# Performance work log

Measured on AMD Instinct MI355X. Metric: run time of the kernel, lower is better.

## Reference

```python
import jax, jax.numpy as jnp
import numpy as np

BATCH = 131072
FEAS = 256
K = 256
DEPTH = 3


def setup_inputs() -> dict:
    key = jax.random.key(0)
    ks = jax.random.split(key, 16)
    # deep tower dims: k//1 -> k//2 -> k//3 -> k//4  == 256 -> 128 -> 85 -> 64
    dims = [K // i for i in range(1, DEPTH + 2)]
    inp = {
        "x": jax.random.normal(ks[0], (BATCH, FEAS), jnp.float32),
        "w_wide": jax.random.normal(ks[1], (FEAS, 1), jnp.float32) * 0.02,
        "b_wide": jnp.zeros((1,), jnp.float32),
        # nn.Parameter(torch.rand(feas, k)) -> uniform [0,1)
        "V": jax.random.uniform(ks[2], (FEAS, K), jnp.float32),
    }
    for i in range(DEPTH):
        fan_in, fan_out = dims[i], dims[i + 1]
        inp[f"w{i+1}"] = jax.random.normal(ks[3 + 2 * i], (fan_in, fan_out), jnp.float32) * (1.0 / np.sqrt(fan_in))
        inp[f"b{i+1}"] = jnp.zeros((fan_out,), jnp.float32)
    inp["w_out"] = jax.random.normal(ks[12], (dims[-1], 1), jnp.float32) * (1.0 / np.sqrt(dims[-1]))
    inp["b_out"] = jnp.zeros((1,), jnp.float32)
    return inp


def reference(x, w_wide, b_wide, V, w1, b1, w2, b2, w3, b3, w_out, b_out):
    # wide (linear) part: [B, 1]
    linear = x @ w_wide + b_wide
    # FM bi-interaction pooling. Original loop: sum_{j >= i} x_i x_j (v_i * v_j)
    # (break/continue on zeros only skip zero-valued terms). Including the
    # diagonal, this equals 0.5 * ((x @ V)^2 + (x^2) @ (V^2)).  [B, K]
    xv = x @ V
    x2v2 = (x * x) @ (V * V)
    tmp = 0.5 * (xv * xv + x2v2)
    # deep tower: Linear + ReLU at each depth
    for w, b in ((w1, b1), (w2, b2), (w3, b3)):
        tmp = jax.nn.relu(tmp @ w + b)
    deep_out = tmp @ w_out + b_out  # [B, 1]
    return jax.nn.sigmoid(linear + deep_out)
```

## Files before the change

### kernel.cpp

```cpp
#include <hip/hip_runtime.h>
#include <math.h>


typedef _Float16 f16;
typedef _Float16 f16x4 __attribute__((ext_vector_type(4)));
typedef _Float16 f16x8 __attribute__((ext_vector_type(8)));
typedef float f32x4 __attribute__((ext_vector_type(4)));

#define NROWS   131072
#define ROWS    64
#define FDIM    256
#define KDIM    256
#define D1      128
#define D2      85
#define D2P     96

#define OFF_VT_H   0x0UL
#define OFF_VT_L   0x20000UL
#define OFF_V2T    0x40000UL
#define OFF_W1T_H  0x60000UL
#define OFF_W1T_L  0x70000UL
#define OFF_W2T_H  0x80000UL
#define OFF_W2T_L  0x86000UL
#define OFF_W3T_H  0x8C000UL
#define OFF_W3T_L  0x8F000UL

static __device__ __forceinline__ f32x4 mfma16(f16x8 a, f16x8 b, f32x4 c) {
  return __builtin_amdgcn_mfma_f32_16x16x32_f16(a, b, c, 0, 0, 0);
}

__global__ __launch_bounds__(256) void prep_kernel(
    const float* __restrict__ V, const float* __restrict__ w1,
    const float* __restrict__ w2, const float* __restrict__ w3,
    f16* VT_h, f16* VT_l, f16* V2T,
    f16* W1T_h, f16* W1T_l, f16* W2T_h, f16* W2T_l, f16* W3T_h, f16* W3T_l) {
  int idx0 = blockIdx.x * 256 + threadIdx.x;
  int stride = gridDim.x * 256;
  for (int idx = idx0; idx < KDIM * FDIM; idx += stride) {
    int k = idx >> 8, i = idx & 255;
    float v = V[i * KDIM + k];
    f16 h = (f16)v;
    VT_h[idx] = h;
    VT_l[idx] = (f16)(v - (float)h);
    V2T[idx] = (f16)(v * v);
  }
  for (int idx = idx0; idx < D1 * KDIM; idx += stride) {
    int n = idx >> 8, k = idx & 255;
    float w = w1[k * D1 + n];
    f16 h = (f16)w;
    W1T_h[idx] = h;
    W1T_l[idx] = (f16)(w - (float)h);
  }
  for (int idx = idx0; idx < D2P * D1; idx += stride) {
    int n = idx >> 7, k = idx & 127;
    float w = (n < D2) ? w2[k * D2 + n] : 0.f;
    f16 h = (f16)w;
    W2T_h[idx] = h;
    W2T_l[idx] = (f16)(w - (float)h);
  }
  for (int idx = idx0; idx < 64 * D2P; idx += stride) {
    int n = idx / D2P, k = idx - n * D2P;
    float w = (k < D2) ? w3[k * 64 + n] : 0.f;
    f16 h = (f16)w;
    W3T_h[idx] = h;
    W3T_l[idx] = (f16)(w - (float)h);
  }
}

__global__ __launch_bounds__(512, 4) void fused_kernel(
    const float* __restrict__ x, const float* __restrict__ w_wide,
    const float* __restrict__ b_wide,
    const f16* __restrict__ VT_h, const f16* __restrict__ VT_l,
    const f16* __restrict__ V2T,
    const f16* __restrict__ W1T_h, const f16* __restrict__ W1T_l,
    const float* __restrict__ b1,
    const f16* __restrict__ W2T_h, const f16* __restrict__ W2T_l,
    const float* __restrict__ b2,
    const f16* __restrict__ W3T_h, const f16* __restrict__ W3T_l,
    const float* __restrict__ b3,
    const float* __restrict__ w_out, const float* __restrict__ b_out,
    float* __restrict__ out) {
  __shared__ __align__(16) f16 smem[32768];
  __shared__ float linS[ROWS];
  __shared__ float pfS[ROWS * 2];

  f16* tmpH = smem;
  f16* tmpL = smem + 16384;
  f16* sXh  = smem;
  f16* sXl  = smem + 2560;
  f16* sX2  = smem + 5120;
  f16* h1H  = smem + 16384;
  f16* h1L  = smem + 24576;
  f16* h2H  = smem;
  f16* h2L  = smem + 8192;

  const int tid = threadIdx.x;
  const int lane = tid & 63, wv = tid >> 6;
  const int q = lane >> 4, ln = lane & 15;
  const int row0 = blockIdx.x * ROWS;
  const int sr = tid >> 3, sc = (tid & 7) * 4;

  f32x4 accV[4][2], acc2[4][2];
#pragma unroll
  for (int i = 0; i < 4; ++i)
#pragma unroll
    for (int j = 0; j < 2; ++j) {
      accV[i][j] = (f32x4){0.f, 0.f, 0.f, 0.f};
      acc2[i][j] = (f32x4){0.f, 0.f, 0.f, 0.f};
    }
  float linp = 0.f;

  const float* xrow = x + (size_t)(row0 + sr) * FDIM + sc;
  float4 a_cur = *(const float4*)(xrow);
  float4 w_cur = *(const float4*)(w_wide + sc);

  for (int ks = 0; ks < 8; ++ks) {
    const int k0 = ks * 32;
    __syncthreads();
    {
      float f0[4] = {a_cur.x, a_cur.y, a_cur.z, a_cur.w};
      f16x4 h0, l0, q0;
#pragma unroll
      for (int j = 0; j < 4; ++j) {
        f16 h = (f16)f0[j];
        h0[j] = h;
        l0[j] = (f16)(f0[j] - (float)h);
        q0[j] = (f16)(f0[j] * f0[j]);
      }
      int off0 = sr * 40 + sc;
      *(f16x4*)(sXh + off0) = h0;
      *(f16x4*)(sXl + off0) = l0;
      *(f16x4*)(sX2 + off0) = q0;
    }
    __syncthreads();

    float4 a_nxt = a_cur, w_nxt = w_cur;
    if (ks < 7) {
      a_nxt = *(const float4*)(xrow + k0 + 32);
      w_nxt = *(const float4*)(w_wide + k0 + 32 + sc);
    }
    linp += a_cur.x * w_cur.x + a_cur.y * w_cur.y + a_cur.z * w_cur.z +
            a_cur.w * w_cur.w;

    f16x8 Bh[2], Bl[2], B2[2];
#pragma unroll
    for (int ni = 0; ni < 2; ++ni) {
      int n = wv * 32 + ni * 16 + ln;
      size_t boff = (size_t)n * FDIM + k0 + q * 8;
      Bh[ni] = *(const f16x8*)(VT_h + boff);
      Bl[ni] = *(const f16x8*)(VT_l + boff);
      B2[ni] = *(const f16x8*)(V2T + boff);
    }
#pragma unroll
    for (int mi = 0; mi < 4; ++mi) {
      int off = (mi * 16 + ln) * 40 + q * 8;
      f16x8 Ah = *(const f16x8*)(sXh + off);
      f16x8 Al = *(const f16x8*)(sXl + off);
      f16x8 A2 = *(const f16x8*)(sX2 + off);
#pragma unroll
      for (int ni = 0; ni < 2; ++ni) {
        accV[mi][ni] = mfma16(Al, Bh[ni], accV[mi][ni]);
        accV[mi][ni] = mfma16(Ah, Bl[ni], accV[mi][ni]);
        accV[mi][ni] = mfma16(Ah, Bh[ni], accV[mi][ni]);
        acc2[mi][ni] = mfma16(A2, B2[ni], acc2[mi][ni]);
      }
    }
    a_cur = a_nxt;
    w_cur = w_nxt;
  }

  {
    float s0 = linp;
    s0 += __shfl_xor(s0, 1);
    s0 += __shfl_xor(s0, 2);
    s0 += __shfl_xor(s0, 4);
    if ((tid & 7) == 0) linS[sr] = s0 + b_wide[0];
  }

  __syncthreads();

#pragma unroll
  for (int mi = 0; mi < 4; ++mi)
#pragma unroll
    for (int r = 0; r < 4; ++r) {
      int m = mi * 16 + q * 4 + r;
      int mrow = m * 256, msw = m & 7;
#pragma unroll
      for (int ni = 0; ni < 2; ++ni) {
        int n = wv * 32 + ni * 16 + ln;
        float xv = accV[mi][ni][r];
        float val = 0.5f * (xv * xv + acc2[mi][ni][r]);
        f16 hi = (f16)val;
        f16 lo = (f16)(val - (float)hi);
        int off = mrow + (((n >> 3) ^ msw) << 3) + (n & 7);
        tmpH[off] = hi;
        tmpL[off] = lo;
      }
    }

  __syncthreads();

  f32x4 acc1[4];
#pragma unroll
  for (int i = 0; i < 4; ++i) acc1[i] = (f32x4){0.f, 0.f, 0.f, 0.f};

#pragma unroll
  for (int ks = 0; ks < 8; ++ks) {
    size_t boff = (size_t)(wv * 16 + ln) * KDIM + ks * 32 + q * 8;
    f16x8 Bh = *(const f16x8*)(W1T_h + boff);
    f16x8 Bl = *(const f16x8*)(W1T_l + boff);
#pragma unroll
    for (int mi = 0; mi < 4; ++mi) {
      int m = mi * 16 + ln;
      int aoff = m * 256 + (((ks * 4 + q) ^ (m & 7)) << 3);
      f16x8 Ah = *(const f16x8*)(tmpH + aoff);
      f16x8 Al = *(const f16x8*)(tmpL + aoff);
      acc1[mi] = mfma16(Al, Bh, acc1[mi]);
      acc1[mi] = mfma16(Ah, Bl, acc1[mi]);
      acc1[mi] = mfma16(Ah, Bh, acc1[mi]);
    }
  }

  __syncthreads();

  {
    int n = wv * 16 + ln;
    float bias = b1[n];
#pragma unroll
    for (int mi = 0; mi < 4; ++mi)
#pragma unroll
      for (int r = 0; r < 4; ++r) {
        int m = mi * 16 + q * 4 + r;
        float z = acc1[mi][r] + bias;
        z = z > 0.f ? z : 0.f;
        f16 hi = (f16)z;
        f16 lo = (f16)(z - (float)hi);
        int off = m * 128 + (((n >> 3) ^ (m & 7)) << 3) + (n & 7);
        h1H[off] = hi;
        h1L[off] = lo;
      }
  }

  __syncthreads();

  const int mt = wv & 3, half = wv >> 2;
  f32x4 accL2[3];
#pragma unroll
  for (int j = 0; j < 3; ++j) accL2[j] = (f32x4){0.f, 0.f, 0.f, 0.f};

#pragma unroll
  for (int ks = 0; ks < 4; ++ks) {
    int m = mt * 16 + ln;
    int aoff = m * 128 + (((ks * 4 + q) ^ (m & 7)) << 3);
    f16x8 Ah = *(const f16x8*)(h1H + aoff);
    f16x8 Al = *(const f16x8*)(h1L + aoff);
#pragma unroll
    for (int nj = 0; nj < 3; ++nj) {
      int n = (half * 3 + nj) * 16 + ln;
      size_t boff = (size_t)n * D1 + ks * 32 + q * 8;
      f16x8 Bh = *(const f16x8*)(W2T_h + boff);
      f16x8 Bl = *(const f16x8*)(W2T_l + boff);
      accL2[nj] = mfma16(Al, Bh, accL2[nj]);
      accL2[nj] = mfma16(Ah, Bl, accL2[nj]);
      accL2[nj] = mfma16(Ah, Bh, accL2[nj]);
    }
  }

#pragma unroll
  for (int r = 0; r < 4; ++r) {
    int m = mt * 16 + q * 4 + r;
    int mrow = m * 128, msw = m & 7;
#pragma unroll
    for (int nj = 0; nj < 3; ++nj) {
      int n = (half * 3 + nj) * 16 + ln;
      float z = accL2[nj][r] + ((n < D2) ? b2[n] : 0.f);
      z = z > 0.f ? z : 0.f;
      f16 hi = (f16)z;
      f16 lo = (f16)(z - (float)hi);
      int off = mrow + (((n >> 3) ^ msw) << 3) + (n & 7);
      h2H[off] = hi;
      h2L[off] = lo;
    }
  }

  __syncthreads();

  f32x4 accL3[2];
  accL3[0] = (f32x4){0.f, 0.f, 0.f, 0.f};
  accL3[1] = (f32x4){0.f, 0.f, 0.f, 0.f};

#pragma unroll
  for (int ks = 0; ks < 3; ++ks) {
    int m = mt * 16 + ln;
    int aoff = m * 128 + (((ks * 4 + q) ^ (m & 7)) << 3);
    f16x8 Ah = *(const f16x8*)(h2H + aoff);
    f16x8 Al = *(const f16x8*)(h2L + aoff);
#pragma unroll
    for (int nj = 0; nj < 2; ++nj) {
      int n = (half * 2 + nj) * 16 + ln;
      size_t boff = (size_t)n * D2P + ks * 32 + q * 8;
      f16x8 Bh = *(const f16x8*)(W3T_h + boff);
      f16x8 Bl = *(const f16x8*)(W3T_l + boff);
      accL3[nj] = mfma16(Al, Bh, accL3[nj]);
      accL3[nj] = mfma16(Ah, Bl, accL3[nj]);
      accL3[nj] = mfma16(Ah, Bh, accL3[nj]);
    }
  }

  {
    float b3v[2], wov[2];
#pragma unroll
    for (int nj = 0; nj < 2; ++nj) {
      int n = (half * 2 + nj) * 16 + ln;
      b3v[nj] = b3[n];
      wov[nj] = w_out[n];
    }
#pragma unroll
    for (int r = 0; r < 4; ++r) {
      float part = 0.f;
#pragma unroll
      for (int nj = 0; nj < 2; ++nj) {
        float z = accL3[nj][r] + b3v[nj];
        part += (z > 0.f ? z : 0.f) * wov[nj];
      }
      part += __shfl_xor(part, 1);
      part += __shfl_xor(part, 2);
      part += __shfl_xor(part, 4);
      part += __shfl_xor(part, 8);
      if (ln == 0) pfS[(mt * 16 + q * 4 + r) * 2 + half] = part;
    }
  }

  __syncthreads();

  if (tid < ROWS) {
    float zf = linS[tid] + pfS[tid * 2] + pfS[tid * 2 + 1] + b_out[0];
    out[row0 + tid] = 1.f / (1.f + expf(-zf));
  }
}

extern "C" void kernel_launch(void* const* d_in, const int* in_sizes, int n_in,
                              void* d_out, int out_size, void* d_ws, size_t ws_size,
                              hipStream_t stream) {
  const float* x = (const float*)d_in[0];
  const float* w_wide = (const float*)d_in[1];
  const float* b_wide = (const float*)d_in[2];
  const float* V = (const float*)d_in[3];
  const float* w1 = (const float*)d_in[4];
  const float* b1 = (const float*)d_in[5];
  const float* w2 = (const float*)d_in[6];
  const float* b2 = (const float*)d_in[7];
  const float* w3 = (const float*)d_in[8];
  const float* b3 = (const float*)d_in[9];
  const float* w_out = (const float*)d_in[10];
  const float* b_out = (const float*)d_in[11];
  float* out = (float*)d_out;
  char* ws = (char*)d_ws;

  f16* VT_h = (f16*)(ws + OFF_VT_H);
  f16* VT_l = (f16*)(ws + OFF_VT_L);
  f16* V2T = (f16*)(ws + OFF_V2T);
  f16* W1T_h = (f16*)(ws + OFF_W1T_H);
  f16* W1T_l = (f16*)(ws + OFF_W1T_L);
  f16* W2T_h = (f16*)(ws + OFF_W2T_H);
  f16* W2T_l = (f16*)(ws + OFF_W2T_L);
  f16* W3T_h = (f16*)(ws + OFF_W3T_H);
  f16* W3T_l = (f16*)(ws + OFF_W3T_L);

  prep_kernel<<<64, 256, 0, stream>>>(V, w1, w2, w3, VT_h, VT_l, V2T, W1T_h,
                                      W1T_l, W2T_h, W2T_l, W3T_h, W3T_l);

  fused_kernel<<<NROWS / ROWS, 512, 0, stream>>>(
      x, w_wide, b_wide, VT_h, VT_l, V2T, W1T_h, W1T_l, b1, W2T_h, W2T_l, b2,
      W3T_h, W3T_l, b3, w_out, b_out, out);
}
```

Baseline: 405.0 us.

## Stage x in 128-wide K chunks to cut barriers in first GEMM

```diff
diff --git a/kernel.cpp b/kernel.cpp
--- a/kernel.cpp
+++ b/kernel.cpp
@@ -14,6 +14,8 @@
 #define D1      128
 #define D2      85
 #define D2P     96
+
+#define SSTRIDE 136
 
 #define OFF_VT_H   0x0UL
 #define OFF_VT_L   0x20000UL
@@ -84,11 +86,11 @@
   __shared__ float linS[ROWS];
   __shared__ float pfS[ROWS * 2];
 
+  f16* sXh  = smem;
+  f16* sXl  = smem + 8704;
+  f16* sX2  = smem + 17408;
   f16* tmpH = smem;
   f16* tmpL = smem + 16384;
-  f16* sXh  = smem;
-  f16* sXl  = smem + 2560;
-  f16* sX2  = smem + 5120;
   f16* h1H  = smem + 16384;
   f16* h1L  = smem + 24576;
   f16* h2H  = smem;
@@ -98,7 +100,7 @@
   const int lane = tid & 63, wv = tid >> 6;
   const int q = lane >> 4, ln = lane & 15;
   const int row0 = blockIdx.x * ROWS;
-  const int sr = tid >> 3, sc = (tid & 7) * 4;
+  const int sr = tid >> 3, sc = (tid & 7) * 16;
 
   f32x4 accV[4][2], acc2[4][2];
 #pragma unroll
@@ -110,15 +112,22 @@
     }
   float linp = 0.f;
 
-  const float* xrow = x + (size_t)(row0 + sr) * FDIM + sc;
-  float4 a_cur = *(const float4*)(xrow);
-  float4 w_cur = *(const float4*)(w_wide + sc);
-
-  for (int ks = 0; ks < 8; ++ks) {
-    const int k0 = ks * 32;
+  for (int kk = 0; kk < 2; ++kk) {
+    const int kbase = kk * 128;
+    float4 a[4], w4[4];
+    const float* xp = x + (size_t)(row0 + sr) * FDIM + kbase + sc;
+    const float* wp = w_wide + kbase + sc;
+#pragma unroll
+    for (int t = 0; t < 4; ++t) {
+      a[t] = *(const float4*)(xp + t * 4);
+      w4[t] = *(const float4*)(wp + t * 4);
+    }
     __syncthreads();
-    {
-      float f0[4] = {a_cur.x, a_cur.y, a_cur.z, a_cur.w};
+#pragma unroll
+    for (int t = 0; t < 4; ++t) {
+      linp += a[t].x * w4[t].x + a[t].y * w4[t].y + a[t].z * w4[t].z +
+              a[t].w * w4[t].w;
+      float f0[4] = {a[t].x, a[t].y, a[t].z, a[t].w};
       f16x4 h0, l0, q0;
 #pragma unroll
       for (int j = 0; j < 4; ++j) {
@@ -127,46 +136,40 @@
         l0[j] = (f16)(f0[j] - (float)h);
         q0[j] = (f16)(f0[j] * f0[j]);
       }
-      int off0 = sr * 40 + sc;
+      int off0 = sr * SSTRIDE + sc + t * 4;
       *(f16x4*)(sXh + off0) = h0;
       *(f16x4*)(sXl + off0) = l0;
       *(f16x4*)(sX2 + off0) = q0;
     }
     __syncthreads();
 
-    float4 a_nxt = a_cur, w_nxt = w_cur;
-    if (ks < 7) {
-      a_nxt = *(const float4*)(xrow + k0 + 32);
-      w_nxt = *(const float4*)(w_wide + k0 + 32 + sc);
-    }
-    linp += a_cur.x * w_cur.x + a_cur.y * w_cur.y + a_cur.z * w_cur.z +
-            a_cur.w * w_cur.w;
-
-    f16x8 Bh[2], Bl[2], B2[2];
-#pragma unroll
-    for (int ni = 0; ni < 2; ++ni) {
-      int n = wv * 32 + ni * 16 + ln;
-      size_t boff = (size_t)n * FDIM + k0 + q * 8;
-      Bh[ni] = *(const f16x8*)(VT_h + boff);
-      Bl[ni] = *(const f16x8*)(VT_l + boff);
-      B2[ni] = *(const f16x8*)(V2T + boff);
-    }
-#pragma unroll
-    for (int mi = 0; mi < 4; ++mi) {
-      int off = (mi * 16 + ln) * 40 + q * 8;
-      f16x8 Ah = *(const f16x8*)(sXh + off);
-      f16x8 Al = *(const f16x8*)(sXl + off);
-      f16x8 A2 = *(const f16x8*)(sX2 + off);
+#pragma unroll
+    for (int ks = 0; ks < 4; ++ks) {
+      const int k0 = kbase + ks * 32;
+      f16x8 Bh[2], Bl[2], B2[2];
 #pragma unroll
       for (int ni = 0; ni < 2; ++ni) {
-        accV[mi][ni] = mfma16(Al, Bh[ni], accV[mi][ni]);
-        accV[mi][ni] = mfma16(Ah, Bl[ni], accV[mi][ni]);
-        accV[mi][ni] = mfma16(Ah, Bh[ni], accV[mi][ni]);
-        acc2[mi][ni] = mfma16(A2, B2[ni], acc2[mi][ni]);
-      }
-    }
-    a_cur = a_nxt;
-    w_cur = w_nxt;
+        int n = wv * 32 + ni * 16 + ln;
+        size_t boff = (size_t)n * FDIM + k0 + q * 8;
+        Bh[ni] = *(const f16x8*)(VT_h + boff);
+        Bl[ni] = *(const f16x8*)(VT_l + boff);
+        B2[ni] = *(const f16x8*)(V2T + boff);
+      }
+#pragma unroll
+      for (int mi = 0; mi < 4; ++mi) {
+        int aoff = (mi * 16 + ln) * SSTRIDE + ks * 32 + q * 8;
+        f16x8 Ah = *(const f16x8*)(sXh + aoff);
+        f16x8 Al = *(const f16x8*)(sXl + aoff);
+        f16x8 A2 = *(const f16x8*)(sX2 + aoff);
+#pragma unroll
+        for (int ni = 0; ni < 2; ++ni) {
+          accV[mi][ni] = mfma16(Al, Bh[ni], accV[mi][ni]);
+          accV[mi][ni] = mfma16(Ah, Bl[ni], accV[mi][ni]);
+          accV[mi][ni] = mfma16(Ah, Bh[ni], accV[mi][ni]);
+          acc2[mi][ni] = mfma16(A2, B2[ni], acc2[mi][ni]);
+        }
+      }
+    }
   }
 
   {
```

New measurement: 398.0 us. No clear change (-1.7%).
